# Kernel tuning notes

Hardware: AMD Instinct MI355X
Metric: run time of the kernel (lower is better)

## Reference

```python
import jax, jax.numpy as jnp
import numpy as np

HID = 512
ALPHA = 0.01
PI = np.float32(np.pi)


def _mlp(x, W0, b0, W1, b1, W2, b2, W3, b3):
    # x: [..., 2] -> scalar field u(x): [...]
    h = jnp.tanh(x @ W0 + b0)
    h = jnp.tanh(h @ W1 + b1)
    h = jnp.tanh(h @ W2 + b2)
    return (h @ W3 + b3)[..., 0]


def _forcing(x):
    # f = -Delta u for u = sin(pi x) sin(pi y^2)
    xx, yy = x[:, 0], x[:, 1]
    return (-PI ** 2 * (1 + 4 * yy ** 2) * jnp.sin(PI * xx) * jnp.sin(PI * yy ** 2)
            + 2 * PI * jnp.sin(PI * xx) * jnp.cos(PI * yy ** 2))


def setup_inputs() -> dict:
    key = jax.random.key(0)
    ks = jax.random.split(key, 6)
    n_i, n_b = 20000, 800
    x_interior = jax.random.uniform(ks[0], (n_i, 2), dtype=jnp.float32)  # domain (0,1)
    theta = jnp.linspace(0.0, 2.0 * np.pi, n_b)
    x_boundary = jnp.stack([(jnp.cos(theta) + 1.0) * 0.5,
                            (jnp.sin(theta) + 1.0) * 0.5], axis=1).astype(jnp.float32)

    def w(k, shape, fan_in):
        return (jax.random.normal(k, shape, jnp.float32) / np.float32(np.sqrt(fan_in)))

    W0 = w(ks[1], (2, HID), 2)
    b0 = jnp.zeros((HID,), jnp.float32)
    W1 = w(ks[2], (HID, HID), HID)
    b1 = jnp.zeros((HID,), jnp.float32)
    W2 = w(ks[3], (HID, HID), HID)
    b2 = jnp.zeros((HID,), jnp.float32)
    W3 = w(ks[4], (HID, 1), HID)
    b3 = jnp.zeros((1,), jnp.float32)
    return dict(x_interior=x_interior, x_boundary=x_boundary,
                W0=W0, b0=b0, W1=W1, b1=b1, W2=W2, b2=b2, W3=W3, b3=b3)


def reference(x_interior, x_boundary, W0, b0, W1, b1, W2, b2, W3, b3):
    params = (W0, b0, W1, b1, W2, b2, W3, b3)

    def u_scalar(x):  # x: [2] -> scalar
        return _mlp(x, *params)

    g = jax.grad(u_scalar)

    def lap_one(x):
        # Laplacian = trace of Hessian via forward-over-reverse HVPs
        lap = jnp.float32(0.0)
        for i in range(2):
            e = jnp.zeros((2,), x.dtype).at[i].set(1.0)
            _, hv = jax.jvp(g, (x,), (e,))
            lap = lap + hv[i]
        return lap

    laplacian = jax.vmap(lap_one)(x_interior)  # [n_interior]
    interior_loss = jnp.mean((laplacian - _forcing(x_interior)) ** 2)
    boundary_loss = jnp.mean(_mlp(x_boundary, *params) ** 2)
    total_loss = ALPHA * interior_loss + boundary_loss
    return total_loss, interior_loss, boundary_loss
```

## Files before the change

kernel.cpp:

```cpp
#include <hip/hip_runtime.h>
#include <math.h>

#define HID 512
#define PPB 16
#define SLAB 512

typedef __attribute__((ext_vector_type(8))) _Float16 half8;
typedef __attribute__((ext_vector_type(4))) _Float16 half4;
typedef __attribute__((ext_vector_type(4))) float f32x4;

static __device__ __forceinline__ float fast_tanh(float x) {
    float e = __expf(2.f * x);
    return 1.f - 2.f / (e + 1.f);
}

__global__ __launch_bounds__(256) void prep_wt(
    const float* __restrict__ W1, const float* __restrict__ W2,
    _Float16* __restrict__ W1h, _Float16* __restrict__ W2h)
{
    __shared__ float T[64][65];
    int b = blockIdx.x;
    const float* W = (b < 64) ? W1 : W2;
    _Float16* Wh   = (b < 64) ? W1h : W2h;
    int tb = b & 63;
    int jbG = tb >> 3, kbG = tb & 7;
    int j0 = jbG * 64, k0 = kbG * 64;
    int t = threadIdx.x;
    #pragma unroll
    for (int r = 0; r < 16; ++r) {
        int kl = r * 4 + (t >> 6);
        int jl = t & 63;
        T[kl][jl] = W[(size_t)(k0 + kl) * HID + j0 + jl];
    }
    __syncthreads();
    int ljb = t >> 6, l15 = (t >> 2) & 15, quad = t & 3;
    #pragma unroll
    for (int lkb = 0; lkb < 2; ++lkb) {
        half8 v;
        #pragma unroll
        for (int k8 = 0; k8 < 8; ++k8)
            v[k8] = (_Float16)T[lkb * 32 + quad * 8 + k8][ljb * 16 + l15];
        size_t out = (size_t)((jbG * 4 + ljb) * 16 + (kbG * 2 + lkb)) * SLAB
                   + l15 * 32 + quad * 8;
        *(half8*)(Wh + out) = v;
    }
}

template<bool FULL>
static __device__ __forceinline__ void layer_pass(
    const _Float16* __restrict__ Wh, const float* __restrict__ bias,
    _Float16* Als, int wv, int lane)
{
    const int l15 = lane & 15, quad = lane >> 4;
    const int j0w = wv * 64;
    const int jb0 = wv * 4;
    const int loff = l15 * 32 + quad * 8;

    f32x4 acc[4][4];
    #pragma unroll
    for (int s = 0; s < 4; ++s)
        #pragma unroll
        for (int jt = 0; jt < 4; ++jt) acc[s][jt] = (f32x4)0.f;

    half8 wA[4], wB[4];
    #pragma unroll
    for (int jt = 0; jt < 4; ++jt)
        wA[jt] = *(const half8*)(Wh + (size_t)((jb0 + jt) * 16) * SLAB + loff);

    auto iter = [&](int kb, half8 (&wc)[4], half8 (&wn)[4]) {
        half8 a[4];
        #pragma unroll
        for (int s = 0; s < 4; ++s)
            a[s] = *(const half8*)(Als + (s * 16 + kb) * SLAB + loff);
        if (kb < 15) {
            #pragma unroll
            for (int jt = 0; jt < 4; ++jt)
                wn[jt] = *(const half8*)(Wh + (size_t)((jb0 + jt) * 16 + kb + 1) * SLAB + loff);
        }
        #pragma unroll
        for (int s = 0; s < 4; ++s)
            #pragma unroll
            for (int jt = 0; jt < 4; ++jt)
                acc[s][jt] = __builtin_amdgcn_mfma_f32_16x16x32_f16(
                    wc[jt], a[s], acc[s][jt], 0, 0, 0);
    };

    #pragma unroll
    for (int kb = 0; kb < 16; kb += 2) {
        iter(kb,     wA, wB);
        iter(kb + 1, wB, wA);
    }

    __syncthreads();

    #pragma unroll
    for (int jt = 0; jt < 4; ++jt) {
        const int jbase = j0w + jt * 16 + quad * 4;
        f32x4 bv = *(const f32x4*)&bias[jbase];
        half4 vh, vt1, vt2, vS;
        #pragma unroll
        for (int r = 0; r < 4; ++r) {
            float a  = fast_tanh(acc[0][jt][r] + bv[r]);
            float g  = 1.f - a * a;
            float z1 = acc[1][jt][r];
            float z2 = acc[2][jt][r];
            vh[r] = (_Float16)a;
            if (FULL) {
                vt1[r] = (_Float16)(g * z1);
                vt2[r] = (_Float16)(g * z2);
            }
            vS[r] = (_Float16)(g * acc[3][jt][r] - 2.f * a * g * (z1 * z1 + z2 * z2));
        }
        const int okb = jbase >> 5;
        const int ooff = l15 * 32 + (jbase & 31);
        *(half4*)(Als + (0 * 16 + okb) * SLAB + ooff) = vh;
        if (FULL) {
            *(half4*)(Als + (1 * 16 + okb) * SLAB + ooff) = vt1;
            *(half4*)(Als + (2 * 16 + okb) * SLAB + ooff) = vt2;
        }
        *(half4*)(Als + (3 * 16 + okb) * SLAB + ooff) = vS;
    }
    __syncthreads();
}

__global__ __launch_bounds__(512, 4) void pois_fused(
    const float* __restrict__ x_int, const float* __restrict__ x_bnd,
    const float* __restrict__ W0, const float* __restrict__ b0,
    const _Float16* __restrict__ W1h, const float* __restrict__ b1,
    const _Float16* __restrict__ W2h, const float* __restrict__ b2,
    const float* __restrict__ W3, const float* __restrict__ b3,
    float* __restrict__ partials, int NI, int NT, int nblk)
{
    __shared__ _Float16 Als[4 * 16 * SLAB];
    __shared__ float sc[32];

    const int tid = threadIdx.x;
    const int wv = tid >> 6, lane = tid & 63;
    const int p0 = blockIdx.x * PPB;

    {
        const int p = lane >> 2, quad = lane & 3;
        int gp = p0 + p;
        int gpc = (gp >= NT) ? 0 : gp;
        float xx, yy;
        if (gpc < NI) { xx = x_int[2 * gpc];        yy = x_int[2 * gpc + 1]; }
        else          { xx = x_bnd[2 * (gpc - NI)]; yy = x_bnd[2 * (gpc - NI) + 1]; }
        #pragma unroll
        for (int i = 0; i < 2; ++i) {
            const int kb = wv * 2 + i;
            const int k = kb * 32 + quad * 8;
            f32x4 w0a = *(const f32x4*)&W0[k],       w0b = *(const f32x4*)&W0[k + 4];
            f32x4 w1a = *(const f32x4*)&W0[HID + k], w1b = *(const f32x4*)&W0[HID + k + 4];
            f32x4 b0a = *(const f32x4*)&b0[k],       b0b = *(const f32x4*)&b0[k + 4];
            half8 vh, vt1, vt2, vS;
            #pragma unroll
            for (int e = 0; e < 8; ++e) {
                float w0i = (e < 4) ? w0a[e] : w0b[e - 4];
                float w1i = (e < 4) ? w1a[e] : w1b[e - 4];
                float bbi = (e < 4) ? b0a[e] : b0b[e - 4];
                float a = fast_tanh(xx * w0i + yy * w1i + bbi);
                float g = 1.f - a * a;
                vh[e]  = (_Float16)a;
                vt1[e] = (_Float16)(g * w0i);
                vt2[e] = (_Float16)(g * w1i);
                vS[e]  = (_Float16)(-2.f * a * g * (w0i * w0i + w1i * w1i));
            }
            const int off = p * 32 + quad * 8;
            *(half8*)(Als + (0 * 16 + kb) * SLAB + off) = vh;
            *(half8*)(Als + (1 * 16 + kb) * SLAB + off) = vt1;
            *(half8*)(Als + (2 * 16 + kb) * SLAB + off) = vt2;
            *(half8*)(Als + (3 * 16 + kb) * SLAB + off) = vS;
        }
    }
    __syncthreads();

    layer_pass<true >(W1h, b1, Als, wv, lane);
    layer_pass<false>(W2h, b2, Als, wv, lane);

    {
        const int hl = lane >> 5, l5 = lane & 31;
        const int p = wv * 2 + hl;
        const int kb = l5 >> 1;
        const int off = p * 32 + (l5 & 1) * 16;
        half8 h0 = *(const half8*)(Als + (0 * 16 + kb) * SLAB + off);
        half8 h1 = *(const half8*)(Als + (0 * 16 + kb) * SLAB + off + 8);
        half8 s0 = *(const half8*)(Als + (3 * 16 + kb) * SLAB + off);
        half8 s1 = *(const half8*)(Als + (3 * 16 + kb) * SLAB + off + 8);
        const int k0 = l5 * 16;
        f32x4 wa = *(const f32x4*)&W3[k0],     wb = *(const f32x4*)&W3[k0 + 4];
        f32x4 wc = *(const f32x4*)&W3[k0 + 8], wd = *(const f32x4*)&W3[k0 + 12];
        float u = 0.f, lap = 0.f;
        #pragma unroll
        for (int e = 0; e < 4; ++e) {
            u   += (float)h0[e] * wa[e] + (float)h0[e + 4] * wb[e]
                 + (float)h1[e] * wc[e] + (float)h1[e + 4] * wd[e];
            lap += (float)s0[e] * wa[e] + (float)s0[e + 4] * wb[e]
                 + (float)s1[e] * wc[e] + (float)s1[e + 4] * wd[e];
        }
        #pragma unroll
        for (int off2 = 1; off2 < 32; off2 <<= 1) {
            u   += __shfl_xor(u, off2);
            lap += __shfl_xor(lap, off2);
        }
        if (l5 == 0) {
            int gp = p0 + p;
            float vi = 0.f, vb = 0.f;
            if (gp < NI) {
                const float PIf = 3.14159265358979323846f;
                float xx = x_int[2 * gp], yy = x_int[2 * gp + 1];
                float sx = sinf(PIf * xx);
                float y2 = yy * yy;
                float sy = sinf(PIf * y2), cy = cosf(PIf * y2);
                float f = -PIf * PIf * (1.f + 4.f * y2) * sx * sy + 2.f * PIf * sx * cy;
                float r = lap - f;
                vi = r * r;
            } else if (gp < NT) {
                float uu = u + b3[0];
                vb = uu * uu;
            }
            sc[p * 2] = vi; sc[p * 2 + 1] = vb;
        }
    }
    __syncthreads();
    if (tid == 0) {
        float svi = 0.f, svb = 0.f;
        #pragma unroll
        for (int p = 0; p < PPB; ++p) { svi += sc[p * 2]; svb += sc[p * 2 + 1]; }
        partials[blockIdx.x] = svi;
        partials[nblk + blockIdx.x] = svb;
    }
}

__global__ __launch_bounds__(256) void pois_reduce(
    const float* __restrict__ partials, float* __restrict__ out,
    int nblk, int NI, int NB)
{
    int tid = threadIdx.x;
    float si = 0.f, sb = 0.f;
    for (int i = tid; i < nblk; i += 256) {
        si += partials[i];
        sb += partials[nblk + i];
    }
    #pragma unroll
    for (int off = 32; off > 0; off >>= 1) {
        si += __shfl_xor(si, off);
        sb += __shfl_xor(sb, off);
    }
    __shared__ float ri[4], rb[4];
    int wv = tid >> 6;
    if ((tid & 63) == 0) { ri[wv] = si; rb[wv] = sb; }
    __syncthreads();
    if (tid == 0) {
        float inter = (ri[0] + ri[1] + ri[2] + ri[3]) / (float)NI;
        float bound = (rb[0] + rb[1] + rb[2] + rb[3]) / (float)NB;
        out[0] = 0.01f * inter + bound;
        out[1] = inter;
        out[2] = bound;
    }
}

extern "C" void kernel_launch(void* const* d_in, const int* in_sizes, int n_in,
                              void* d_out, int out_size, void* d_ws, size_t ws_size,
                              hipStream_t stream)
{
    const float* x_int = (const float*)d_in[0];
    const float* x_bnd = (const float*)d_in[1];
    const float* W0 = (const float*)d_in[2];
    const float* b0 = (const float*)d_in[3];
    const float* W1 = (const float*)d_in[4];
    const float* b1 = (const float*)d_in[5];
    const float* W2 = (const float*)d_in[6];
    const float* b2 = (const float*)d_in[7];
    const float* W3 = (const float*)d_in[8];
    const float* b3 = (const float*)d_in[9];

    int NI = in_sizes[0] / 2;
    int NB = in_sizes[1] / 2;
    int NT = NI + NB;
    int nblk = (NT + PPB - 1) / PPB;

    float* partials = (float*)d_ws;
    _Float16* W1h = (_Float16*)((char*)d_ws + 16384);
    _Float16* W2h = W1h + 262144;

    prep_wt<<<128, 256, 0, stream>>>(W1, W2, W1h, W2h);

    pois_fused<<<nblk, 512, 0, stream>>>(
        x_int, x_bnd, W0, b0, W1h, b1, W2h, b2, W3, b3,
        partials, NI, NT, nblk);

    pois_reduce<<<1, 256, 0, stream>>>(partials, (float*)d_out, nblk, NI, NB);
}
```

Measured before the change: 193.7 us.

## Relayout LDS fragments for contiguous lane access and fuse final reduction via atomic counter

Changes the shared-memory and packed-weight fragment layout so each lane reads a contiguous 8-half chunk (lane*8), aimed at removing LDS bank conflicts on the MFMA operand loads. The output-layer reduction is restructured so each wave handles its own k-blocks and the per-point sums are combined across waves in shared memory, instead of a 32-lane shuffle tree. The separate reduce kernel is dropped: the last block, found through an atomic counter reset in prep_wt, performs the global reduction. This saves one launch but adds an atomic and threadfences per block.

```diff
diff --git a/kernel.cpp b/kernel.cpp
--- a/kernel.cpp
+++ b/kernel.cpp
@@ -14,12 +14,15 @@
     return 1.f - 2.f / (e + 1.f);
 }
 
+
 __global__ __launch_bounds__(256) void prep_wt(
     const float* __restrict__ W1, const float* __restrict__ W2,
-    _Float16* __restrict__ W1h, _Float16* __restrict__ W2h)
+    _Float16* __restrict__ W1h, _Float16* __restrict__ W2h,
+    int* __restrict__ counter)
 {
     __shared__ float T[64][65];
     int b = blockIdx.x;
+    if (b == 0 && threadIdx.x == 0) *counter = 0;
     const float* W = (b < 64) ? W1 : W2;
     _Float16* Wh   = (b < 64) ? W1h : W2h;
     int tb = b & 63;
@@ -33,7 +36,9 @@
         T[kl][jl] = W[(size_t)(k0 + kl) * HID + j0 + jl];
     }
     __syncthreads();
-    int ljb = t >> 6, l15 = (t >> 2) & 15, quad = t & 3;
+    int ljb = t >> 6;
+    int l15 = (t >> 2) & 15;
+    int quad = t & 3;
     #pragma unroll
     for (int lkb = 0; lkb < 2; ++lkb) {
         half8 v;
@@ -41,7 +46,7 @@
         for (int k8 = 0; k8 < 8; ++k8)
             v[k8] = (_Float16)T[lkb * 32 + quad * 8 + k8][ljb * 16 + l15];
         size_t out = (size_t)((jbG * 4 + ljb) * 16 + (kbG * 2 + lkb)) * SLAB
-                   + l15 * 32 + quad * 8;
+                   + (quad * 16 + l15) * 8;
         *(half8*)(Wh + out) = v;
     }
 }
@@ -54,7 +59,7 @@
     const int l15 = lane & 15, quad = lane >> 4;
     const int j0w = wv * 64;
     const int jb0 = wv * 4;
-    const int loff = l15 * 32 + quad * 8;
+    const int loff = lane * 8;
 
     f32x4 acc[4][4];
     #pragma unroll
@@ -112,7 +117,8 @@
             vS[r] = (_Float16)(g * acc[3][jt][r] - 2.f * a * g * (z1 * z1 + z2 * z2));
         }
         const int okb = jbase >> 5;
-        const int ooff = l15 * 32 + (jbase & 31);
+        const int qo  = (jbase & 31) >> 3;
+        const int ooff = (qo * 16 + l15) * 8 + (jbase & 7);
         *(half4*)(Als + (0 * 16 + okb) * SLAB + ooff) = vh;
         if (FULL) {
             *(half4*)(Als + (1 * 16 + okb) * SLAB + ooff) = vt1;
@@ -129,17 +135,19 @@
     const _Float16* __restrict__ W1h, const float* __restrict__ b1,
     const _Float16* __restrict__ W2h, const float* __restrict__ b2,
     const float* __restrict__ W3, const float* __restrict__ b3,
-    float* __restrict__ partials, int NI, int NT, int nblk)
+    float* __restrict__ partials, int* __restrict__ counter,
+    float* __restrict__ out, int NI, int NT, int nblk)
 {
     __shared__ _Float16 Als[4 * 16 * SLAB];
-    __shared__ float sc[32];
+    __shared__ float scU[8][16], scL[8][16], sc[32];
+    __shared__ int isLast;
 
     const int tid = threadIdx.x;
     const int wv = tid >> 6, lane = tid & 63;
     const int p0 = blockIdx.x * PPB;
 
     {
-        const int p = lane >> 2, quad = lane & 3;
+        const int p = lane & 15, quad = lane >> 4;
         int gp = p0 + p;
         int gpc = (gp >= NT) ? 0 : gp;
         float xx, yy;
@@ -165,7 +173,7 @@
                 vt2[e] = (_Float16)(g * w1i);
                 vS[e]  = (_Float16)(-2.f * a * g * (w0i * w0i + w1i * w1i));
             }
-            const int off = p * 32 + quad * 8;
+            const int off = lane * 8;
             *(half8*)(Als + (0 * 16 + kb) * SLAB + off) = vh;
             *(half8*)(Als + (1 * 16 + kb) * SLAB + off) = vt1;
             *(half8*)(Als + (2 * 16 + kb) * SLAB + off) = vt2;
@@ -178,48 +186,47 @@
     layer_pass<false>(W2h, b2, Als, wv, lane);
 
     {
-        const int hl = lane >> 5, l5 = lane & 31;
-        const int p = wv * 2 + hl;
-        const int kb = l5 >> 1;
-        const int off = p * 32 + (l5 & 1) * 16;
-        half8 h0 = *(const half8*)(Als + (0 * 16 + kb) * SLAB + off);
-        half8 h1 = *(const half8*)(Als + (0 * 16 + kb) * SLAB + off + 8);
-        half8 s0 = *(const half8*)(Als + (3 * 16 + kb) * SLAB + off);
-        half8 s1 = *(const half8*)(Als + (3 * 16 + kb) * SLAB + off + 8);
-        const int k0 = l5 * 16;
-        f32x4 wa = *(const f32x4*)&W3[k0],     wb = *(const f32x4*)&W3[k0 + 4];
-        f32x4 wc = *(const f32x4*)&W3[k0 + 8], wd = *(const f32x4*)&W3[k0 + 12];
+        const int p = lane & 15, quad = lane >> 4;
         float u = 0.f, lap = 0.f;
         #pragma unroll
-        for (int e = 0; e < 4; ++e) {
-            u   += (float)h0[e] * wa[e] + (float)h0[e + 4] * wb[e]
-                 + (float)h1[e] * wc[e] + (float)h1[e + 4] * wd[e];
-            lap += (float)s0[e] * wa[e] + (float)s0[e + 4] * wb[e]
-                 + (float)s1[e] * wc[e] + (float)s1[e + 4] * wd[e];
-        }
-        #pragma unroll
-        for (int off2 = 1; off2 < 32; off2 <<= 1) {
-            u   += __shfl_xor(u, off2);
-            lap += __shfl_xor(lap, off2);
-        }
-        if (l5 == 0) {
-            int gp = p0 + p;
-            float vi = 0.f, vb = 0.f;
-            if (gp < NI) {
-                const float PIf = 3.14159265358979323846f;
-                float xx = x_int[2 * gp], yy = x_int[2 * gp + 1];
-                float sx = sinf(PIf * xx);
-                float y2 = yy * yy;
-                float sy = sinf(PIf * y2), cy = cosf(PIf * y2);
-                float f = -PIf * PIf * (1.f + 4.f * y2) * sx * sy + 2.f * PIf * sx * cy;
-                float r = lap - f;
-                vi = r * r;
-            } else if (gp < NT) {
-                float uu = u + b3[0];
-                vb = uu * uu;
+        for (int i = 0; i < 2; ++i) {
+            const int kb = wv * 2 + i;
+            const int k = kb * 32 + quad * 8;
+            half8 hh = *(const half8*)(Als + (0 * 16 + kb) * SLAB + lane * 8);
+            half8 ss = *(const half8*)(Als + (3 * 16 + kb) * SLAB + lane * 8);
+            f32x4 wa = *(const f32x4*)&W3[k], wb = *(const f32x4*)&W3[k + 4];
+            #pragma unroll
+            for (int e = 0; e < 4; ++e) {
+                u   += (float)hh[e] * wa[e] + (float)hh[e + 4] * wb[e];
+                lap += (float)ss[e] * wa[e] + (float)ss[e + 4] * wb[e];
             }
-            sc[p * 2] = vi; sc[p * 2 + 1] = vb;
-        }
+        }
+        u   += __shfl_xor(u, 16);   u   += __shfl_xor(u, 32);
+        lap += __shfl_xor(lap, 16); lap += __shfl_xor(lap, 32);
+        if (lane < 16) { scU[wv][lane] = u; scL[wv][lane] = lap; }
+    }
+    __syncthreads();
+    if (tid < 16) {
+        const int p = tid;
+        float u = 0.f, lap = 0.f;
+        #pragma unroll
+        for (int w = 0; w < 8; ++w) { u += scU[w][p]; lap += scL[w][p]; }
+        int gp = p0 + p;
+        float vi = 0.f, vb = 0.f;
+        if (gp < NI) {
+            const float PIf = 3.14159265358979323846f;
+            float xx = x_int[2 * gp], yy = x_int[2 * gp + 1];
+            float sx = sinf(PIf * xx);
+            float y2 = yy * yy;
+            float sy = sinf(PIf * y2), cy = cosf(PIf * y2);
+            float f = -PIf * PIf * (1.f + 4.f * y2) * sx * sy + 2.f * PIf * sx * cy;
+            float r = lap - f;
+            vi = r * r;
+        } else if (gp < NT) {
+            float uu = u + b3[0];
+            vb = uu * uu;
+        }
+        sc[p * 2] = vi; sc[p * 2 + 1] = vb;
     }
     __syncthreads();
     if (tid == 0) {
@@ -228,34 +235,37 @@
         for (int p = 0; p < PPB; ++p) { svi += sc[p * 2]; svb += sc[p * 2 + 1]; }
         partials[blockIdx.x] = svi;
         partials[nblk + blockIdx.x] = svb;
-    }
-}
-
-__global__ __launch_bounds__(256) void pois_reduce(
-    const float* __restrict__ partials, float* __restrict__ out,
-    int nblk, int NI, int NB)
-{
-    int tid = threadIdx.x;
-    float si = 0.f, sb = 0.f;
-    for (int i = tid; i < nblk; i += 256) {
-        si += partials[i];
-        sb += partials[nblk + i];
-    }
-    #pragma unroll
-    for (int off = 32; off > 0; off >>= 1) {
-        si += __shfl_xor(si, off);
-        sb += __shfl_xor(sb, off);
-    }
-    __shared__ float ri[4], rb[4];
-    int wv = tid >> 6;
-    if ((tid & 63) == 0) { ri[wv] = si; rb[wv] = sb; }
-    __syncthreads();
-    if (tid == 0) {
-        float inter = (ri[0] + ri[1] + ri[2] + ri[3]) / (float)NI;
-        float bound = (rb[0] + rb[1] + rb[2] + rb[3]) / (float)NB;
-        out[0] = 0.01f * inter + bound;
-        out[1] = inter;
-        out[2] = bound;
+        __threadfence();
+        int t = atomicAdd(counter, 1);
+        isLast = (t == nblk - 1);
+    }
+    __syncthreads();
+
+    if (isLast) {
+        __threadfence();
+        float si = 0.f, sb = 0.f;
+        for (int i = tid; i < nblk; i += 512) {
+            si += partials[i];
+            sb += partials[nblk + i];
+        }
+        #pragma unroll
+        for (int off = 32; off > 0; off >>= 1) {
+            si += __shfl_xor(si, off);
+            sb += __shfl_xor(sb, off);
+        }
+        __shared__ float ri[8], rb[8];
+        if (lane == 0) { ri[wv] = si; rb[wv] = sb; }
+        __syncthreads();
+        if (tid == 0) {
+            float ti = 0.f, tb = 0.f;
+            #pragma unroll
+            for (int w = 0; w < 8; ++w) { ti += ri[w]; tb += rb[w]; }
+            float inter = ti / (float)NI;
+            float bound = tb / (float)(NT - NI);
+            out[0] = 0.01f * inter + bound;
+            out[1] = inter;
+            out[2] = bound;
+        }
     }
 }
 
@@ -278,16 +288,16 @@
     int NB = in_sizes[1] / 2;
     int NT = NI + NB;
     int nblk = (NT + PPB - 1) / PPB;
+    (void)NB;
 
     float* partials = (float*)d_ws;
+    int* counter = (int*)((char*)d_ws + 12800);
     _Float16* W1h = (_Float16*)((char*)d_ws + 16384);
     _Float16* W2h = W1h + 262144;
 
-    prep_wt<<<128, 256, 0, stream>>>(W1, W2, W1h, W2h);
+    prep_wt<<<128, 256, 0, stream>>>(W1, W2, W1h, W2h, counter);
 
     pois_fused<<<nblk, 512, 0, stream>>>(
         x_int, x_bnd, W0, b0, W1h, b1, W2h, b2, W3, b3,
-        partials, NI, NT, nblk);
-
-    pois_reduce<<<1, 256, 0, stream>>>(partials, (float*)d_out, nblk, NI, NB);
-}
+        partials, counter, (float*)d_out, NI, NT, nblk);
+}
```

New measurement: 197.4 us. About the same (+1.9%).

## Double points per block to 32 with 16 waves and lane-contiguous fragment layout

Applied to the files above, without the earlier changes.

Raises points per block from 16 to 32 and threads per block from 512 to 1024 (16 waves), so each wave computes 32 output columns for two point-groups. Each weight fragment loaded from global memory now feeds MFMAs for twice as many points, which halves weight traffic per point. The LDS fragment layout becomes lane-contiguous (lane*8) to simplify addressing, and the final dot-product reduction is split across waves through shared memory. The block now needs twice the LDS (128KB of activations), so fewer blocks fit per CU, and the launch bound of 1024 threads with 4 blocks cannot actually be met.

```diff
diff --git a/kernel.cpp b/kernel.cpp
--- a/kernel.cpp
+++ b/kernel.cpp
@@ -2,7 +2,7 @@
 #include <math.h>
 
 #define HID 512
-#define PPB 16
+#define PPB 32
 #define SLAB 512
 
 typedef __attribute__((ext_vector_type(8))) _Float16 half8;
@@ -13,6 +13,7 @@
     float e = __expf(2.f * x);
     return 1.f - 2.f / (e + 1.f);
 }
+
 
 __global__ __launch_bounds__(256) void prep_wt(
     const float* __restrict__ W1, const float* __restrict__ W2,
@@ -33,7 +34,9 @@
         T[kl][jl] = W[(size_t)(k0 + kl) * HID + j0 + jl];
     }
     __syncthreads();
-    int ljb = t >> 6, l15 = (t >> 2) & 15, quad = t & 3;
+    int ljb = t >> 6;
+    int l15 = (t >> 2) & 15;
+    int quad = t & 3;
     #pragma unroll
     for (int lkb = 0; lkb < 2; ++lkb) {
         half8 v;
@@ -41,7 +44,7 @@
         for (int k8 = 0; k8 < 8; ++k8)
             v[k8] = (_Float16)T[lkb * 32 + quad * 8 + k8][ljb * 16 + l15];
         size_t out = (size_t)((jbG * 4 + ljb) * 16 + (kbG * 2 + lkb)) * SLAB
-                   + l15 * 32 + quad * 8;
+                   + (quad * 16 + l15) * 8;
         *(half8*)(Wh + out) = v;
     }
 }
@@ -52,37 +55,42 @@
     _Float16* Als, int wv, int lane)
 {
     const int l15 = lane & 15, quad = lane >> 4;
-    const int j0w = wv * 64;
-    const int jb0 = wv * 4;
-    const int loff = l15 * 32 + quad * 8;
-
-    f32x4 acc[4][4];
+    const int j0w = wv * 32;
+    const int jb0 = wv * 2;
+    const int loff = lane * 8;
+
+    f32x4 acc[4][2][2];
     #pragma unroll
     for (int s = 0; s < 4; ++s)
         #pragma unroll
-        for (int jt = 0; jt < 4; ++jt) acc[s][jt] = (f32x4)0.f;
-
-    half8 wA[4], wB[4];
-    #pragma unroll
-    for (int jt = 0; jt < 4; ++jt)
+        for (int pf = 0; pf < 2; ++pf)
+            #pragma unroll
+            for (int jt = 0; jt < 2; ++jt) acc[s][pf][jt] = (f32x4)0.f;
+
+    half8 wA[2], wB[2];
+    #pragma unroll
+    for (int jt = 0; jt < 2; ++jt)
         wA[jt] = *(const half8*)(Wh + (size_t)((jb0 + jt) * 16) * SLAB + loff);
 
-    auto iter = [&](int kb, half8 (&wc)[4], half8 (&wn)[4]) {
-        half8 a[4];
-        #pragma unroll
-        for (int s = 0; s < 4; ++s)
-            a[s] = *(const half8*)(Als + (s * 16 + kb) * SLAB + loff);
+    auto iter = [&](int kb, half8 (&wc)[2], half8 (&wn)[2]) {
         if (kb < 15) {
             #pragma unroll
-            for (int jt = 0; jt < 4; ++jt)
+            for (int jt = 0; jt < 2; ++jt)
                 wn[jt] = *(const half8*)(Wh + (size_t)((jb0 + jt) * 16 + kb + 1) * SLAB + loff);
         }
         #pragma unroll
-        for (int s = 0; s < 4; ++s)
-            #pragma unroll
-            for (int jt = 0; jt < 4; ++jt)
-                acc[s][jt] = __builtin_amdgcn_mfma_f32_16x16x32_f16(
-                    wc[jt], a[s], acc[s][jt], 0, 0, 0);
+        for (int pf = 0; pf < 2; ++pf) {
+            half8 a[4];
+            #pragma unroll
+            for (int s = 0; s < 4; ++s)
+                a[s] = *(const half8*)(Als + ((s * 2 + pf) * 16 + kb) * SLAB + loff);
+            #pragma unroll
+            for (int s = 0; s < 4; ++s)
+                #pragma unroll
+                for (int jt = 0; jt < 2; ++jt)
+                    acc[s][pf][jt] = __builtin_amdgcn_mfma_f32_16x16x32_f16(
+                        wc[jt], a[s], acc[s][pf][jt], 0, 0, 0);
+        }
     };
 
     #pragma unroll
@@ -94,36 +102,40 @@
     __syncthreads();
 
     #pragma unroll
-    for (int jt = 0; jt < 4; ++jt) {
+    for (int jt = 0; jt < 2; ++jt) {
         const int jbase = j0w + jt * 16 + quad * 4;
+        const int qo = jt * 2 + (quad >> 1);
+        const int e0 = (quad & 1) * 4;
         f32x4 bv = *(const f32x4*)&bias[jbase];
-        half4 vh, vt1, vt2, vS;
-        #pragma unroll
-        for (int r = 0; r < 4; ++r) {
-            float a  = fast_tanh(acc[0][jt][r] + bv[r]);
-            float g  = 1.f - a * a;
-            float z1 = acc[1][jt][r];
-            float z2 = acc[2][jt][r];
-            vh[r] = (_Float16)a;
+        #pragma unroll
+        for (int pf = 0; pf < 2; ++pf) {
+            half4 vh, vt1, vt2, vS;
+            #pragma unroll
+            for (int r = 0; r < 4; ++r) {
+                float a  = fast_tanh(acc[0][pf][jt][r] + bv[r]);
+                float g  = 1.f - a * a;
+                float z1 = acc[1][pf][jt][r];
+                float z2 = acc[2][pf][jt][r];
+                vh[r] = (_Float16)a;
+                if (FULL) {
+                    vt1[r] = (_Float16)(g * z1);
+                    vt2[r] = (_Float16)(g * z2);
+                }
+                vS[r] = (_Float16)(g * acc[3][pf][jt][r] - 2.f * a * g * (z1 * z1 + z2 * z2));
+            }
+            const int ooff = (qo * 16 + l15) * 8 + e0;
+            *(half4*)(Als + ((0 * 2 + pf) * 16 + wv) * SLAB + ooff) = vh;
             if (FULL) {
-                vt1[r] = (_Float16)(g * z1);
-                vt2[r] = (_Float16)(g * z2);
+                *(half4*)(Als + ((1 * 2 + pf) * 16 + wv) * SLAB + ooff) = vt1;
+                *(half4*)(Als + ((2 * 2 + pf) * 16 + wv) * SLAB + ooff) = vt2;
             }
-            vS[r] = (_Float16)(g * acc[3][jt][r] - 2.f * a * g * (z1 * z1 + z2 * z2));
-        }
-        const int okb = jbase >> 5;
-        const int ooff = l15 * 32 + (jbase & 31);
-        *(half4*)(Als + (0 * 16 + okb) * SLAB + ooff) = vh;
-        if (FULL) {
-            *(half4*)(Als + (1 * 16 + okb) * SLAB + ooff) = vt1;
-            *(half4*)(Als + (2 * 16 + okb) * SLAB + ooff) = vt2;
-        }
-        *(half4*)(Als + (3 * 16 + okb) * SLAB + ooff) = vS;
-    }
-    __syncthreads();
-}
-
-__global__ __launch_bounds__(512, 4) void pois_fused(
+            *(half4*)(Als + ((3 * 2 + pf) * 16 + wv) * SLAB + ooff) = vS;
+        }
+    }
+    __syncthreads();
+}
+
+__global__ __launch_bounds__(1024, 4) void pois_fused(
     const float* __restrict__ x_int, const float* __restrict__ x_bnd,
     const float* __restrict__ W0, const float* __restrict__ b0,
     const _Float16* __restrict__ W1h, const float* __restrict__ b1,
@@ -131,46 +143,44 @@
     const float* __restrict__ W3, const float* __restrict__ b3,
     float* __restrict__ partials, int NI, int NT, int nblk)
 {
-    __shared__ _Float16 Als[4 * 16 * SLAB];
-    __shared__ float sc[32];
+    __shared__ _Float16 Als[8 * 16 * SLAB];
+    __shared__ float scU[16][32], scL[16][32], sc[64];
 
     const int tid = threadIdx.x;
     const int wv = tid >> 6, lane = tid & 63;
+    const int l15 = lane & 15, quad = lane >> 4;
     const int p0 = blockIdx.x * PPB;
 
-    {
-        const int p = lane >> 2, quad = lane & 3;
+    #pragma unroll
+    for (int ph = 0; ph < 2; ++ph) {
+        const int p = ph * 16 + l15;
         int gp = p0 + p;
         int gpc = (gp >= NT) ? 0 : gp;
         float xx, yy;
         if (gpc < NI) { xx = x_int[2 * gpc];        yy = x_int[2 * gpc + 1]; }
         else          { xx = x_bnd[2 * (gpc - NI)]; yy = x_bnd[2 * (gpc - NI) + 1]; }
-        #pragma unroll
-        for (int i = 0; i < 2; ++i) {
-            const int kb = wv * 2 + i;
-            const int k = kb * 32 + quad * 8;
-            f32x4 w0a = *(const f32x4*)&W0[k],       w0b = *(const f32x4*)&W0[k + 4];
-            f32x4 w1a = *(const f32x4*)&W0[HID + k], w1b = *(const f32x4*)&W0[HID + k + 4];
-            f32x4 b0a = *(const f32x4*)&b0[k],       b0b = *(const f32x4*)&b0[k + 4];
-            half8 vh, vt1, vt2, vS;
-            #pragma unroll
-            for (int e = 0; e < 8; ++e) {
-                float w0i = (e < 4) ? w0a[e] : w0b[e - 4];
-                float w1i = (e < 4) ? w1a[e] : w1b[e - 4];
-                float bbi = (e < 4) ? b0a[e] : b0b[e - 4];
-                float a = fast_tanh(xx * w0i + yy * w1i + bbi);
-                float g = 1.f - a * a;
-                vh[e]  = (_Float16)a;
-                vt1[e] = (_Float16)(g * w0i);
-                vt2[e] = (_Float16)(g * w1i);
-                vS[e]  = (_Float16)(-2.f * a * g * (w0i * w0i + w1i * w1i));
-            }
-            const int off = p * 32 + quad * 8;
-            *(half8*)(Als + (0 * 16 + kb) * SLAB + off) = vh;
-            *(half8*)(Als + (1 * 16 + kb) * SLAB + off) = vt1;
-            *(half8*)(Als + (2 * 16 + kb) * SLAB + off) = vt2;
-            *(half8*)(Als + (3 * 16 + kb) * SLAB + off) = vS;
-        }
+        const int k = wv * 32 + quad * 8;
+        f32x4 w0a = *(const f32x4*)&W0[k],       w0b = *(const f32x4*)&W0[k + 4];
+        f32x4 w1a = *(const f32x4*)&W0[HID + k], w1b = *(const f32x4*)&W0[HID + k + 4];
+        f32x4 b0a = *(const f32x4*)&b0[k],       b0b = *(const f32x4*)&b0[k + 4];
+        half8 vh, vt1, vt2, vS;
+        #pragma unroll
+        for (int e = 0; e < 8; ++e) {
+            float w0i = (e < 4) ? w0a[e] : w0b[e - 4];
+            float w1i = (e < 4) ? w1a[e] : w1b[e - 4];
+            float bbi = (e < 4) ? b0a[e] : b0b[e - 4];
+            float a = fast_tanh(xx * w0i + yy * w1i + bbi);
+            float g = 1.f - a * a;
+            vh[e]  = (_Float16)a;
+            vt1[e] = (_Float16)(g * w0i);
+            vt2[e] = (_Float16)(g * w1i);
+            vS[e]  = (_Float16)(-2.f * a * g * (w0i * w0i + w1i * w1i));
+        }
+        const int off = lane * 8;
+        *(half8*)(Als + ((0 * 2 + ph) * 16 + wv) * SLAB + off) = vh;
+        *(half8*)(Als + ((1 * 2 + ph) * 16 + wv) * SLAB + off) = vt1;
+        *(half8*)(Als + ((2 * 2 + ph) * 16 + wv) * SLAB + off) = vt2;
+        *(half8*)(Als + ((3 * 2 + ph) * 16 + wv) * SLAB + off) = vS;
     }
     __syncthreads();
 
@@ -178,48 +188,45 @@
     layer_pass<false>(W2h, b2, Als, wv, lane);
 
     {
-        const int hl = lane >> 5, l5 = lane & 31;
-        const int p = wv * 2 + hl;
-        const int kb = l5 >> 1;
-        const int off = p * 32 + (l5 & 1) * 16;
-        half8 h0 = *(const half8*)(Als + (0 * 16 + kb) * SLAB + off);
-        half8 h1 = *(const half8*)(Als + (0 * 16 + kb) * SLAB + off + 8);
-        half8 s0 = *(const half8*)(Als + (3 * 16 + kb) * SLAB + off);
-        half8 s1 = *(const half8*)(Als + (3 * 16 + kb) * SLAB + off + 8);
-        const int k0 = l5 * 16;
-        f32x4 wa = *(const f32x4*)&W3[k0],     wb = *(const f32x4*)&W3[k0 + 4];
-        f32x4 wc = *(const f32x4*)&W3[k0 + 8], wd = *(const f32x4*)&W3[k0 + 12];
+        const int k = wv * 32 + quad * 8;
+        f32x4 wa = *(const f32x4*)&W3[k], wb = *(const f32x4*)&W3[k + 4];
+        #pragma unroll
+        for (int ph = 0; ph < 2; ++ph) {
+            half8 hh = *(const half8*)(Als + ((0 * 2 + ph) * 16 + wv) * SLAB + lane * 8);
+            half8 ss = *(const half8*)(Als + ((3 * 2 + ph) * 16 + wv) * SLAB + lane * 8);
+            float u = 0.f, lap = 0.f;
+            #pragma unroll
+            for (int e = 0; e < 4; ++e) {
+                u   += (float)hh[e] * wa[e] + (float)hh[e + 4] * wb[e];
+                lap += (float)ss[e] * wa[e] + (float)ss[e + 4] * wb[e];
+            }
+            u   += __shfl_xor(u, 16);   u   += __shfl_xor(u, 32);
+            lap += __shfl_xor(lap, 16); lap += __shfl_xor(lap, 32);
+            if (lane < 16) { scU[wv][ph * 16 + lane] = u; scL[wv][ph * 16 + lane] = lap; }
+        }
+    }
+    __syncthreads();
+    if (tid < 32) {
+        const int p = tid;
         float u = 0.f, lap = 0.f;
         #pragma unroll
-        for (int e = 0; e < 4; ++e) {
-            u   += (float)h0[e] * wa[e] + (float)h0[e + 4] * wb[e]
-                 + (float)h1[e] * wc[e] + (float)h1[e + 4] * wd[e];
-            lap += (float)s0[e] * wa[e] + (float)s0[e + 4] * wb[e]
-                 + (float)s1[e] * wc[e] + (float)s1[e + 4] * wd[e];
-        }
-        #pragma unroll
-        for (int off2 = 1; off2 < 32; off2 <<= 1) {
-            u   += __shfl_xor(u, off2);
-            lap += __shfl_xor(lap, off2);
-        }
-        if (l5 == 0) {
-            int gp = p0 + p;
-            float vi = 0.f, vb = 0.f;
-            if (gp < NI) {
-                const float PIf = 3.14159265358979323846f;
-                float xx = x_int[2 * gp], yy = x_int[2 * gp + 1];
-                float sx = sinf(PIf * xx);
-                float y2 = yy * yy;
-                float sy = sinf(PIf * y2), cy = cosf(PIf * y2);
-                float f = -PIf * PIf * (1.f + 4.f * y2) * sx * sy + 2.f * PIf * sx * cy;
-                float r = lap - f;
-                vi = r * r;
-            } else if (gp < NT) {
-                float uu = u + b3[0];
-                vb = uu * uu;
-            }
-            sc[p * 2] = vi; sc[p * 2 + 1] = vb;
-        }
+        for (int w = 0; w < 16; ++w) { u += scU[w][p]; lap += scL[w][p]; }
+        int gp = p0 + p;
+        float vi = 0.f, vb = 0.f;
+        if (gp < NI) {
+            const float PIf = 3.14159265358979323846f;
+            float xx = x_int[2 * gp], yy = x_int[2 * gp + 1];
+            float sx = sinf(PIf * xx);
+            float y2 = yy * yy;
+            float sy = sinf(PIf * y2), cy = cosf(PIf * y2);
+            float f = -PIf * PIf * (1.f + 4.f * y2) * sx * sy + 2.f * PIf * sx * cy;
+            float r = lap - f;
+            vi = r * r;
+        } else if (gp < NT) {
+            float uu = u + b3[0];
+            vb = uu * uu;
+        }
+        sc[p * 2] = vi; sc[p * 2 + 1] = vb;
     }
     __syncthreads();
     if (tid == 0) {
@@ -285,7 +292,7 @@
 
     prep_wt<<<128, 256, 0, stream>>>(W1, W2, W1h, W2h);
 
-    pois_fused<<<nblk, 512, 0, stream>>>(
+    pois_fused<<<nblk, 1024, 0, stream>>>(
         x_int, x_bnd, W0, b0, W1h, b1, W2h, b2, W3, b3,
         partials, NI, NT, nblk);
 
```

After: 173.7 us. 1.12x faster.
